# Kernel optimization log

Hardware: AMD Instinct MI355X
Metric: run time of the kernel (lower is better)

## Reference

```python
import jax, jax.numpy as jnp
import numpy as np

L, H, P = 8192, 1024, 512
DT_MIN, DT_MAX = 1e-3, 1e-1
CONJ_SYM = True


def setup_inputs() -> dict:
    key = jax.random.key(0)
    ks = jax.random.split(key, 6)
    input_sequence = jax.random.normal(ks[0], (L, H), jnp.float32)
    # HiPPO-DPLR-like eigenvalues: negative real part, linearly spaced imag part
    Lambda_re = -0.5 * jnp.ones((P,), jnp.float32)
    Lambda_im = jnp.pi * jnp.arange(P, dtype=jnp.float32)
    # B param stacks real/imag in last dim: (P, H, 2); C: (H, P, 2)
    B = jax.random.normal(ks[1], (P, H, 2), jnp.float32) / np.float32(np.sqrt(2 * H))
    C = jax.random.normal(ks[2], (H, P, 2), jnp.float32) / np.float32(np.sqrt(2 * P))
    D = jax.random.normal(ks[3], (H,), jnp.float32)
    log_step = jax.random.uniform(ks[4], (P,), jnp.float32,
                                  minval=np.float32(np.log(DT_MIN)),
                                  maxval=np.float32(np.log(DT_MAX)))
    return dict(input_sequence=input_sequence, Lambda_re=Lambda_re,
                Lambda_im=Lambda_im, B=B, C=C, D=D, log_step=log_step)


def _binop(e_i, e_j):
    # diagonal LTI composition: (A, b) o (A', b') = (A'A, A'b + b')
    A_i, b_i = e_i
    A_j, b_j = e_j
    return A_j * A_i, A_j * b_i + b_j


def _forward(input_sequence, Lambda_re, Lambda_im, B, C, D, log_step):
    Lambda = Lambda_re + 1j * Lambda_im                  # (P,) complex
    B_tilde = B[..., 0] + 1j * B[..., 1]                 # (P, H)
    C_tilde = C[..., 0] + 1j * C[..., 1]                 # (H, P)
    step = jnp.exp(log_step)                             # (P,)  step_rescale = 1.0
    # ZOH discretization
    Lambda_bar = jnp.exp(Lambda * step)                  # (P,)
    B_bar = ((1.0 / Lambda) * (Lambda_bar - 1.0))[:, None] * B_tilde  # (P, H)
    # input projection, vectorized over L: Bu[l] = B_bar @ u[l]
    Bu = input_sequence.astype(B_bar.dtype) @ B_bar.T    # (L, P) complex
    Lambda_elems = jnp.broadcast_to(Lambda_bar, Bu.shape)  # (L, P)
    _, xs = jax.lax.associative_scan(_binop, (Lambda_elems, Bu))  # states (L, P)
    mult = 2.0 if CONJ_SYM else 1.0
    ys = mult * jnp.einsum('lp,hp->lh', xs, C_tilde).real  # (L, H)
    out = ys + D * input_sequence                          # D-skip
    return out, xs[-1]


def reference(input_sequence, Lambda_re, Lambda_im, B, C, D, log_step):
    return _forward(input_sequence, Lambda_re, Lambda_im, B, C, D, log_step)
```

## Files before the change

### kernel.cpp

```cpp
#include <hip/hip_runtime.h>
#include <hip/hip_bf16.h>
#include <hip/hip_fp16.h>
#include <stdint.h>

typedef _Float16 f16;
typedef __attribute__((ext_vector_type(8))) _Float16 half8;
typedef __attribute__((ext_vector_type(4))) _Float16 half4;
typedef __attribute__((ext_vector_type(4))) float f32x4;

#define L_SEQ 8192
#define H_DIM 1024
#define P_DIM 512
#define NB 256
#define TT 32

#define GL16(gp, lp)                                                        \
  __builtin_amdgcn_global_load_lds(                                          \
      (const __attribute__((address_space(1))) void*)(gp),                   \
      (__attribute__((address_space(3))) void*)(lp), 16, 0, 0)


__global__ void k_prep(const float* __restrict__ B, const float* __restrict__ C,
                       const float* __restrict__ u, const float* __restrict__ lre,
                       const float* __restrict__ lim, const float* __restrict__ lstp,
                       float* __restrict__ cst, f16* __restrict__ W1,
                       f16* __restrict__ W2, f16* __restrict__ uh) {
  int blk = blockIdx.x;
  if (blk < 4096) {
    int idx = blk * 256 + threadIdx.x;
    int n = idx >> 10, k = idx & 1023;
    int p = n >> 1;
    double step = exp((double)lstp[p]);
    double ar = (double)lre[p] * step, ai = (double)lim[p] * step;
    double er = exp(ar);
    double lbr = er * cos(ai), lbi = er * sin(ai);
    double nr = lbr - 1.0, ni = lbi;
    double d = (double)lre[p] * (double)lre[p] + (double)lim[p] * (double)lim[p];
    double gr = (nr * (double)lre[p] + ni * (double)lim[p]) / d;
    double gi = (ni * (double)lre[p] - nr * (double)lim[p]) / d;
    int e = ilogb(fmax(fabs(gr), fabs(gi))) + 1;
    float inv = ldexpf(1.0f, -e);
    float grf = (float)gr, gif = (float)gi;
    float b0 = B[(size_t)(p * 1024 + k) * 2];
    float b1 = B[(size_t)(p * 1024 + k) * 2 + 1];
    float re = (grf * b0 - gif * b1) * inv;
    float im = (grf * b1 + gif * b0) * inv;
    W1[idx] = (f16)((n & 1) ? im : re);
  } else if (blk < 8192) {
    int idx = (blk - 4096) * 256 + threadIdx.x;
    int h = idx >> 10, k = idx & 1023;
    int p = k >> 1;
    float v = (k & 1) ? -2.0f * C[(size_t)(h * 512 + p) * 2 + 1]
                      :  2.0f * C[(size_t)(h * 512 + p) * 2];
    W2[idx] = (f16)v;
  } else if (blk < 16384) {
    int i = (blk - 8192) * 256 + threadIdx.x;
    float4 v = reinterpret_cast<const float4*>(u)[i];
    half4 h;
    h.x = (f16)v.x; h.y = (f16)v.y; h.z = (f16)v.z; h.w = (f16)v.w;
    reinterpret_cast<half4*>(uh)[i] = h;
  } else {
    int t = threadIdx.x;
    if (t < 64) {
      int p = (blk - 16384) * 64 + t;
      double step = exp((double)lstp[p]);
      double ar = (double)lre[p] * step, ai = (double)lim[p] * step;
      double er = exp(ar);
      double lbr = er * cos(ai), lbi = er * sin(ai);
      cst[p] = (float)lbr; cst[512 + p] = (float)lbi;
      double e32 = exp(ar * 32.0);
      double pr = e32 * cos(ai * 32.0), pi = e32 * sin(ai * 32.0);
#pragma unroll
      for (int s = 0; s < 8; ++s) {
        cst[3072 + s * 1024 + p]       = (float)pr;
        cst[3072 + s * 1024 + 512 + p] = (float)pi;
        double nr2 = pr * pr - pi * pi, ni2 = 2.0 * pr * pi;
        pr = nr2; pi = ni2;
      }
      double nr = lbr - 1.0, ni = lbi;
      double d = (double)lre[p] * (double)lre[p] + (double)lim[p] * (double)lim[p];
      double gr = (nr * (double)lre[p] + ni * (double)lim[p]) / d;
      double gi = (ni * (double)lre[p] - nr * (double)lim[p]) / d;
      int e = ilogb(fmax(fabs(gr), fabs(gi))) + 1;
      float sc = ldexpf(1.0f, e);
      cst[11264 + 2 * p] = sc;
      cst[11264 + 2 * p + 1] = sc;
    }
  }
}

template <int EPI>
__global__ __launch_bounds__(256) void k_gemm(const f16* __restrict__ A,
                                              const f16* __restrict__ Bm,
                                              float* __restrict__ CmF,
                                              f16* __restrict__ CmH,
                                              const float* __restrict__ D,
                                              const f16* __restrict__ Uh,
                                              const float* __restrict__ S) {
  __shared__ f16 As[128 * 64];
  __shared__ f16 Bs[128 * 64];
  const int tid = threadIdx.x;
  const int wave = tid >> 6, lane = tid & 63;
  const int bm = blockIdx.x >> 3, bn = blockIdx.x & 7;
  const int m0 = bm * 128, n0 = bn * 128;
  const int wr = (wave >> 1) * 64, wc = (wave & 1) * 64;
  const int lr = lane & 15, lg = lane >> 4;
  f32x4 acc[4][4] = {};

  int srow[4], scol[4];
#pragma unroll
  for (int w = 0; w < 4; ++w) {
    int c = w * 256 + tid;
    srow[w] = c >> 3;
    scol[w] = ((c & 7) * 8) ^ ((srow[w] & 7) << 3);
  }

  for (int kt = 0; kt < 16; ++kt) {
    const int k0 = kt * 64;
#pragma unroll
    for (int w = 0; w < 4; ++w) {
      GL16(A + (size_t)(m0 + srow[w]) * 1024 + k0 + scol[w],
           (char*)As + (w * 256 + wave * 64) * 16);
      GL16(Bm + (size_t)(n0 + srow[w]) * 1024 + k0 + scol[w],
           (char*)Bs + (w * 256 + wave * 64) * 16);
    }
    __syncthreads();
    half8 af[2][4], bf[2][4];
#pragma unroll
    for (int m = 0; m < 4; ++m) {
      int ra = wr + m * 16 + lr;
      int sw = (ra & 7) << 4;
      af[0][m] = *(const half8*)((const char*)As + ra * 128 + ((lg * 16) ^ sw));
      af[1][m] = *(const half8*)((const char*)As + ra * 128 + ((64 + lg * 16) ^ sw));
    }
#pragma unroll
    for (int n = 0; n < 4; ++n) {
      int rb = wc + n * 16 + lr;
      int sw = (rb & 7) << 4;
      bf[0][n] = *(const half8*)((const char*)Bs + rb * 128 + ((lg * 16) ^ sw));
      bf[1][n] = *(const half8*)((const char*)Bs + rb * 128 + ((64 + lg * 16) ^ sw));
    }
#pragma unroll
    for (int h = 0; h < 2; ++h)
#pragma unroll
      for (int m = 0; m < 4; ++m)
#pragma unroll
        for (int n = 0; n < 4; ++n)
          acc[m][n] = __builtin_amdgcn_mfma_f32_16x16x32_f16(af[h][m], bf[h][n], acc[m][n], 0, 0, 0);
    __syncthreads();
  }

#pragma unroll
  for (int m = 0; m < 4; ++m)
#pragma unroll
    for (int n = 0; n < 4; ++n) {
      int row = m0 + wr + m * 16 + lg * 4;
      int col = n0 + wc + n * 16 + lr;
      float scale = (EPI == 0) ? S[col] : 0.0f;
#pragma unroll
      for (int j = 0; j < 4; ++j) {
        float v = acc[m][n][j];
        if (EPI) {
          v += D[col] * (float)Uh[(size_t)(row + j) * 1024 + col];
          CmF[(size_t)(row + j) * 1024 + col] = v;
        } else {
          CmH[(size_t)(row + j) * 1024 + col] = (f16)(v * scale);
        }
      }
    }
}

__global__ void k_scanA(const f16* __restrict__ Bu, const float* __restrict__ cst,
                        float* __restrict__ carry) {
  int p = threadIdx.x;
  int b = blockIdx.x;
  float lbr = cst[p], lbi = cst[512 + p];
  float xr = 0.f, xi = 0.f;
  const uint32_t* row32 = (const uint32_t*)(Bu + (size_t)b * TT * 1024);
#pragma unroll
  for (int t = 0; t < TT; ++t) {
    union { uint32_t u; f16 h[2]; } cv;
    cv.u = row32[t * 512 + p];
    float br = (float)cv.h[0], bi = (float)cv.h[1];
    float nxr = lbr * xr - lbi * xi + br;
    float nxi = lbr * xi + lbi * xr + bi;
    xr = nxr; xi = nxi;
  }
  carry[b * 1024 + p] = xr;
  carry[b * 1024 + 512 + p] = xi;
}

__global__ void k_scanB(const float* __restrict__ carry, const float* __restrict__ cst,
                        float* __restrict__ prefix) {
  __shared__ float sre[256], sim[256];
  int p = blockIdx.x;
  int b = threadIdx.x;
  float xr = carry[b * 1024 + p], xi = carry[b * 1024 + 512 + p];
  sre[b] = xr; sim[b] = xi;
  __syncthreads();
#pragma unroll
  for (int s = 0; s < 8; ++s) {
    float pr = cst[3072 + s * 1024 + p];
    float pi = cst[3072 + s * 1024 + 512 + p];
    int off = 1 << s;
    float ar = 0.f, ai = 0.f;
    if (b >= off) { ar = sre[b - off]; ai = sim[b - off]; }
    __syncthreads();
    xr += pr * ar - pi * ai;
    xi += pr * ai + pi * ar;
    sre[b] = xr; sim[b] = xi;
    __syncthreads();
  }
  float er = 0.f, ei = 0.f;
  if (b > 0) { er = sre[b - 1]; ei = sim[b - 1]; }
  prefix[b * 1024 + p] = er;
  prefix[b * 1024 + 512 + p] = ei;
}

__global__ void k_scanC(const f16* __restrict__ Bu, const float* __restrict__ cst,
                        const float* __restrict__ prefix, f16* __restrict__ X,
                        float* __restrict__ fin, int tail) {
  int p = threadIdx.x;
  int b = blockIdx.x;
  float lbr = cst[p], lbi = cst[512 + p];
  float xr = prefix[b * 1024 + p], xi = prefix[b * 1024 + 512 + p];
  const uint32_t* row32 = (const uint32_t*)(Bu + (size_t)b * TT * 1024);
  uint32_t* xrow32 = (uint32_t*)(X + (size_t)b * TT * 1024);
#pragma unroll
  for (int t = 0; t < TT; ++t) {
    union { uint32_t u; f16 h[2]; } cv;
    cv.u = row32[t * 512 + p];
    float br = (float)cv.h[0], bi = (float)cv.h[1];
    float nxr = lbr * xr - lbi * xi + br;
    float nxi = lbr * xi + lbi * xr + bi;
    xr = nxr; xi = nxi;
    union { uint32_t u; f16 h[2]; } ov;
    ov.h[0] = (f16)xr; ov.h[1] = (f16)xi;
    xrow32[t * 512 + p] = ov.u;
  }
  if (b == NB - 1) {
    if (tail >= 1024) {
      fin[2 * p] = xr;
      fin[2 * p + 1] = xi;
    } else if (tail >= 512) {
      fin[p] = xr;
    }
  }
}

extern "C" void kernel_launch(void* const* d_in, const int* in_sizes, int n_in,
                              void* d_out, int out_size, void* d_ws, size_t ws_size,
                              hipStream_t stream) {
  const float* u    = (const float*)d_in[0];
  const float* lre  = (const float*)d_in[1];
  const float* lim  = (const float*)d_in[2];
  const float* B    = (const float*)d_in[3];
  const float* C    = (const float*)d_in[4];
  const float* D    = (const float*)d_in[5];
  const float* lstp = (const float*)d_in[6];
  float* out = (float*)d_out;
  int tail = out_size - L_SEQ * H_DIM;

  char* ws = (char*)d_ws;
  float* cst   = (float*)(ws + 0);
  f16* uh      = (f16*)(ws + 65536);
  f16* W1      = (f16*)(ws + 16842752);
  f16* W2      = (f16*)(ws + 18939904);
  f16* Bu      = (f16*)(ws + 21037056);
  f16* Xc      = (f16*)(ws + 37814272);
  float* carry = (float*)(ws + 54591488);
  float* prefix= (float*)(ws + 55639040);

  k_prep<<<16392, 256, 0, stream>>>(B, C, u, lre, lim, lstp, cst, W1, W2, uh);
  k_gemm<0><<<512, 256, 0, stream>>>(uh, W1, nullptr, Bu, nullptr, nullptr, cst + 11264);
  k_scanA<<<NB, 512, 0, stream>>>(Bu, cst, carry);
  k_scanB<<<512, 256, 0, stream>>>(carry, cst, prefix);
  k_scanC<<<NB, 512, 0, stream>>>(Bu, cst, prefix, Xc, out + (size_t)L_SEQ * H_DIM, tail);
  k_gemm<1><<<512, 256, 0, stream>>>(Xc, W2, out, nullptr, D, uh, nullptr);
}
```

Before: 176.0 us.

## Double-buffer GEMM LDS tiles, swizzle block order, hoist per-block prep constants

The GEMM kernel now uses two LDS buffers and issues the global-to-LDS loads for the next K tile before computing on the current one, so memory latency can overlap MFMA work. Block indices are remapped so that consecutive blocks share B column tiles, which should improve L2 reuse. In the prep kernel, the double-precision discretization constants are computed once per block by thread 0 and shared through LDS instead of by every thread. Doubling LDS to 64KB per block may reduce occupancy.

```diff
diff --git a/kernel.cpp b/kernel.cpp
--- a/kernel.cpp
+++ b/kernel.cpp
@@ -25,22 +25,26 @@
                        const float* __restrict__ lim, const float* __restrict__ lstp,
                        float* __restrict__ cst, f16* __restrict__ W1,
                        f16* __restrict__ W2, f16* __restrict__ uh) {
+  __shared__ float sg[3];
   int blk = blockIdx.x;
   if (blk < 4096) {
     int idx = blk * 256 + threadIdx.x;
     int n = idx >> 10, k = idx & 1023;
     int p = n >> 1;
-    double step = exp((double)lstp[p]);
-    double ar = (double)lre[p] * step, ai = (double)lim[p] * step;
-    double er = exp(ar);
-    double lbr = er * cos(ai), lbi = er * sin(ai);
-    double nr = lbr - 1.0, ni = lbi;
-    double d = (double)lre[p] * (double)lre[p] + (double)lim[p] * (double)lim[p];
-    double gr = (nr * (double)lre[p] + ni * (double)lim[p]) / d;
-    double gi = (ni * (double)lre[p] - nr * (double)lim[p]) / d;
-    int e = ilogb(fmax(fabs(gr), fabs(gi))) + 1;
-    float inv = ldexpf(1.0f, -e);
-    float grf = (float)gr, gif = (float)gi;
+    if (threadIdx.x == 0) {
+      double step = exp((double)lstp[p]);
+      double ar = (double)lre[p] * step, ai = (double)lim[p] * step;
+      double er = exp(ar);
+      double lbr = er * cos(ai), lbi = er * sin(ai);
+      double nr = lbr - 1.0, ni = lbi;
+      double d = (double)lre[p] * (double)lre[p] + (double)lim[p] * (double)lim[p];
+      double gr = (nr * (double)lre[p] + ni * (double)lim[p]) / d;
+      double gi = (ni * (double)lre[p] - nr * (double)lim[p]) / d;
+      int e = ilogb(fmax(fabs(gr), fabs(gi))) + 1;
+      sg[0] = (float)gr; sg[1] = (float)gi; sg[2] = ldexpf(1.0f, -e);
+    }
+    __syncthreads();
+    float grf = sg[0], gif = sg[1], inv = sg[2];
     float b0 = B[(size_t)(p * 1024 + k) * 2];
     float b1 = B[(size_t)(p * 1024 + k) * 2 + 1];
     float re = (grf * b0 - gif * b1) * inv;
@@ -97,11 +101,13 @@
                                               const float* __restrict__ D,
                                               const f16* __restrict__ Uh,
                                               const float* __restrict__ S) {
-  __shared__ f16 As[128 * 64];
-  __shared__ f16 Bs[128 * 64];
+  __shared__ f16 As[2][128 * 64];
+  __shared__ f16 Bs[2][128 * 64];
   const int tid = threadIdx.x;
   const int wave = tid >> 6, lane = tid & 63;
-  const int bm = blockIdx.x >> 3, bn = blockIdx.x & 7;
+  const int bid = blockIdx.x;
+  const int swz = (bid & 7) * 64 + (bid >> 3);
+  const int bm = swz >> 3, bn = swz & 7;
   const int m0 = bm * 128, n0 = bn * 128;
   const int wr = (wave >> 1) * 64, wc = (wave & 1) * 64;
   const int lr = lane & 15, lg = lane >> 4;
@@ -115,30 +121,40 @@
     scol[w] = ((c & 7) * 8) ^ ((srow[w] & 7) << 3);
   }
 
+#define STAGE(buf, kt)                                                        \
+  {                                                                           \
+    const int k0 = (kt) * 64;                                                 \
+    _Pragma("unroll")                                                         \
+    for (int w = 0; w < 4; ++w) {                                             \
+      GL16(A + (size_t)(m0 + srow[w]) * 1024 + k0 + scol[w],                  \
+           (char*)&As[buf][0] + (w * 256 + wave * 64) * 16);                  \
+      GL16(Bm + (size_t)(n0 + srow[w]) * 1024 + k0 + scol[w],                 \
+           (char*)&Bs[buf][0] + (w * 256 + wave * 64) * 16);                  \
+    }                                                                         \
+  }
+
+  STAGE(0, 0);
+  __syncthreads();
+
   for (int kt = 0; kt < 16; ++kt) {
-    const int k0 = kt * 64;
-#pragma unroll
-    for (int w = 0; w < 4; ++w) {
-      GL16(A + (size_t)(m0 + srow[w]) * 1024 + k0 + scol[w],
-           (char*)As + (w * 256 + wave * 64) * 16);
-      GL16(Bm + (size_t)(n0 + srow[w]) * 1024 + k0 + scol[w],
-           (char*)Bs + (w * 256 + wave * 64) * 16);
-    }
-    __syncthreads();
+    const int cur = kt & 1;
+    if (kt < 15) STAGE(cur ^ 1, kt + 1);
+    const char* pa = (const char*)&As[cur][0];
+    const char* pb = (const char*)&Bs[cur][0];
     half8 af[2][4], bf[2][4];
 #pragma unroll
     for (int m = 0; m < 4; ++m) {
       int ra = wr + m * 16 + lr;
       int sw = (ra & 7) << 4;
-      af[0][m] = *(const half8*)((const char*)As + ra * 128 + ((lg * 16) ^ sw));
-      af[1][m] = *(const half8*)((const char*)As + ra * 128 + ((64 + lg * 16) ^ sw));
+      af[0][m] = *(const half8*)(pa + ra * 128 + ((lg * 16) ^ sw));
+      af[1][m] = *(const half8*)(pa + ra * 128 + ((64 + lg * 16) ^ sw));
     }
 #pragma unroll
     for (int n = 0; n < 4; ++n) {
       int rb = wc + n * 16 + lr;
       int sw = (rb & 7) << 4;
-      bf[0][n] = *(const half8*)((const char*)Bs + rb * 128 + ((lg * 16) ^ sw));
-      bf[1][n] = *(const half8*)((const char*)Bs + rb * 128 + ((64 + lg * 16) ^ sw));
+      bf[0][n] = *(const half8*)(pb + rb * 128 + ((lg * 16) ^ sw));
+      bf[1][n] = *(const half8*)(pb + rb * 128 + ((64 + lg * 16) ^ sw));
     }
 #pragma unroll
     for (int h = 0; h < 2; ++h)
@@ -149,6 +165,7 @@
           acc[m][n] = __builtin_amdgcn_mfma_f32_16x16x32_f16(af[h][m], bf[h][n], acc[m][n], 0, 0, 0);
     __syncthreads();
   }
+#undef STAGE
 
 #pragma unroll
   for (int m = 0; m < 4; ++m)
```

Result: faster. 166.9 us (-5.2%).
